# Optimization experiments

Hardware: AMD Instinct MI355X
Metric: run time of the kernel (lower is better)

The kernel has to match this reference:

```python
import jax, jax.numpy as jnp
import numpy as np

D_MODEL = 1024
NUM_HEADS = 16
HEAD_DIM = D_MODEL // NUM_HEADS
EPS = 1e-06


def setup_inputs() -> dict:
    key = jax.random.key(0)
    ks = jax.random.split(key, 7)
    B, T, D = 4, 4096, D_MODEL
    scale = 1.0 / np.sqrt(D)
    x = jax.random.normal(ks[0], (B, T, D), dtype=jnp.float32)
    Wq = jax.random.normal(ks[1], (D, D), dtype=jnp.float32) * scale
    Wk = jax.random.normal(ks[2], (D, D), dtype=jnp.float32) * scale
    Wv = jax.random.normal(ks[3], (D, D), dtype=jnp.float32) * scale
    Wo = jax.random.normal(ks[4], (D, D), dtype=jnp.float32) * scale
    Wg = jax.random.normal(ks[5], (D, D), dtype=jnp.float32) * scale
    bg = jnp.zeros((D,), dtype=jnp.float32)
    return {"x": x, "Wq": Wq, "Wk": Wk, "Wv": Wv, "Wo": Wo, "Wg": Wg, "bg": bg}


def phi(x):
    return jax.nn.elu(x) + 1.0


def reference(x, Wq, Wk, Wv, Wo, Wg, bg):
    B, T, D = x.shape
    H, Hd = NUM_HEADS, HEAD_DIM
    # torch nn.Linear: y = x @ W.T
    q = phi((x @ Wq.T).reshape(B, T, H, Hd))
    k = phi((x @ Wk.T).reshape(B, T, H, Hd))
    v = (x @ Wv.T).reshape(B, T, H, Hd)
    k_sum = k.sum(axis=1)                              # [B,H,Hd]
    kv_sum = jnp.einsum('bthd,bthd->bhd', k, v)        # [B,H,Hd] (elementwise-product reduction, as in source)
    # out[b,t,h,v] = sum_d q[b,t,h,d]*kv_sum[b,h,d], identical for every v
    s = jnp.einsum('bthd,bhd->bth', q, kv_sum)         # [B,T,H]
    z = jnp.einsum('bthd,bhd->bth', q, k_sum) + EPS    # [B,T,H]
    out = (s / z)[..., None] * jnp.ones((Hd,), dtype=x.dtype)  # broadcast over head_dim
    out = out.reshape(B, T, D)
    gate = jax.nn.sigmoid(x @ Wg.T + bg)
    return gate * out + (1.0 - gate) * x
```

## Files before the change

### kernel.cpp

```cpp
#include <hip/hip_runtime.h>

#define D_MODEL 1024
#define TSEQ    4096
#define BATCH   4
#define MROWS   (BATCH * TSEQ)
#define KDIM    1024
#define NDIM    1024
#define EPSV    1e-6f

typedef __attribute__((ext_vector_type(8))) short short8;
typedef __attribute__((ext_vector_type(4))) float floatx4;

__device__ inline unsigned short f2bf(float f) {
  unsigned u = __float_as_uint(f);
  unsigned r = (u + 0x7FFFu + ((u >> 16) & 1u)) >> 16;
  return (unsigned short)r;
}
__device__ inline float bf2f(unsigned short h) {
  return __uint_as_float(((unsigned)h) << 16);
}
__device__ inline float phi_f(float x) { return x > 0.f ? x + 1.f : __expf(x); }

#define NX4 4194304
#define NW4 262144
#define NZ4 2048

__global__ __launch_bounds__(256) void prep_kernel(
    const float* __restrict__ x,  const float* __restrict__ wq,
    const float* __restrict__ wk, const float* __restrict__ wv,
    const float* __restrict__ wg,
    unsigned short* __restrict__ xb,  unsigned short* __restrict__ wqb,
    unsigned short* __restrict__ wkb, unsigned short* __restrict__ wvb,
    unsigned short* __restrict__ wgb, float* __restrict__ zbase)
{
  long i = (long)blockIdx.x * 256 + threadIdx.x;
  const float* src; unsigned short* dst; long j = i;
  if (j < NX4) { src = x; dst = xb; }
  else {
    j -= NX4;
    if (j < NW4) { src = wq; dst = wqb; }
    else { j -= NW4;
      if (j < NW4) { src = wk; dst = wkb; }
      else { j -= NW4;
        if (j < NW4) { src = wv; dst = wvb; }
        else { j -= NW4;
          if (j < NW4) { src = wg; dst = wgb; }
          else { j -= NW4;
            if (j < NZ4) { float4 zz = {0.f,0.f,0.f,0.f}; ((float4*)zbase)[j] = zz; }
            return;
          }
        }
      }
    }
  }
  float4 f = ((const float4*)src)[j];
  ushort4 o;
  o.x = f2bf(f.x); o.y = f2bf(f.y); o.z = f2bf(f.z); o.w = f2bf(f.w);
  ((ushort4*)dst)[j] = o;
}

#define BM 128
#define BN 128
#define BK 32

__global__ __launch_bounds__(256, 2) void gemm_kv_kernel(
    const unsigned short* __restrict__ A,
    const unsigned short* __restrict__ Wk, const unsigned short* __restrict__ Wv,
    float* __restrict__ ksum, float* __restrict__ kvsum)
{
  const int bn = blockIdx.x;
  const int bm = blockIdx.y;

  __shared__ __align__(16) unsigned short As[BM * BK];
  __shared__ __align__(16) unsigned short Bk[BN * BK];
  __shared__ __align__(16) unsigned short Bv[BN * BK];

  const int tid  = threadIdx.x;
  const int lane = tid & 63;
  const int w    = tid >> 6;
  const int wr   = (w >> 1) * 64;
  const int wc   = (w & 1) * 64;

  floatx4 ak[4][4], av[4][4];
#pragma unroll
  for (int i = 0; i < 4; i++)
#pragma unroll
    for (int j = 0; j < 4; j++) {
      floatx4 zz = {0.f,0.f,0.f,0.f}; ak[i][j] = zz; av[i][j] = zz;
    }

  const unsigned short* Ablk  = A  + (size_t)bm * BM * KDIM;
  const unsigned short* Bkblk = Wk + (size_t)bn * BN * KDIM;
  const unsigned short* Bvblk = Wv + (size_t)bn * BN * KDIM;

  const int la = lane & 15;
  const int lk = (lane >> 4) * 8;

  for (int kt = 0; kt < KDIM; kt += BK) {
    __syncthreads();
#pragma unroll
    for (int c = 0; c < 2; c++) {
      int f   = tid + c * 256;
      int row = f >> 2;
      int col = (f & 3) * 8;
      size_t goff = (size_t)row * KDIM + kt + col;
      __builtin_amdgcn_global_load_lds(
          (const __attribute__((address_space(1))) void*)(Ablk + goff),
          (__attribute__((address_space(3))) void*)(As + (size_t)f * 8), 16, 0, 0);
      __builtin_amdgcn_global_load_lds(
          (const __attribute__((address_space(1))) void*)(Bkblk + goff),
          (__attribute__((address_space(3))) void*)(Bk + (size_t)f * 8), 16, 0, 0);
      __builtin_amdgcn_global_load_lds(
          (const __attribute__((address_space(1))) void*)(Bvblk + goff),
          (__attribute__((address_space(3))) void*)(Bv + (size_t)f * 8), 16, 0, 0);
    }
    __syncthreads();

    short8 af[4], bk[4], bv[4];
#pragma unroll
    for (int i = 0; i < 4; i++) {
      af[i] = *(const short8*)&As[(wr + i * 16 + la) * BK + lk];
      bk[i] = *(const short8*)&Bk[(wc + i * 16 + la) * BK + lk];
      bv[i] = *(const short8*)&Bv[(wc + i * 16 + la) * BK + lk];
    }
#pragma unroll
    for (int i = 0; i < 4; i++)
#pragma unroll
      for (int j = 0; j < 4; j++) {
        ak[i][j] = __builtin_amdgcn_mfma_f32_16x16x32_bf16(af[i], bk[j], ak[i][j], 0, 0, 0);
        av[i][j] = __builtin_amdgcn_mfma_f32_16x16x32_bf16(af[i], bv[j], av[i][j], 0, 0, 0);
      }
  }

  const int b = bm >> 5;
  float kp[4] = {0.f,0.f,0.f,0.f};
  float vp[4] = {0.f,0.f,0.f,0.f};
#pragma unroll
  for (int j = 0; j < 4; j++)
#pragma unroll
    for (int i = 0; i < 4; i++)
#pragma unroll
      for (int r = 0; r < 4; r++) {
        float kk = phi_f(ak[i][j][r]);
        kp[j] += kk;
        vp[j] += kk * av[i][j][r];
      }
#pragma unroll
  for (int j = 0; j < 4; j++) {
    kp[j] += __shfl_xor(kp[j], 16, 64); kp[j] += __shfl_xor(kp[j], 32, 64);
    vp[j] += __shfl_xor(vp[j], 16, 64); vp[j] += __shfl_xor(vp[j], 32, 64);
  }
  if (lane < 16) {
#pragma unroll
    for (int j = 0; j < 4; j++) {
      int col = bn * BN + wc + j * 16 + lane;
      atomicAdd(ksum  + (size_t)b * D_MODEL + col, kp[j]);
      atomicAdd(kvsum + (size_t)b * D_MODEL + col, vp[j]);
    }
  }
}

__global__ __launch_bounds__(512) void gemm_qg_kernel(
    const unsigned short* __restrict__ A,
    const unsigned short* __restrict__ Wq, const unsigned short* __restrict__ Wg,
    const float* __restrict__ x, const float* __restrict__ bg,
    const float* __restrict__ ksum, const float* __restrict__ kvsum,
    float* __restrict__ out)
{
  const int bn = blockIdx.x;
  const int bm = blockIdx.y;

  __shared__ __align__(16) unsigned short As[BM * BK];
  __shared__ __align__(16) unsigned short Bq[BN * BK];
  __shared__ __align__(16) unsigned short Bg[BN * BK];
  __shared__ float o_lds[2 * BM];

  const int tid  = threadIdx.x;
  const int lane = tid & 63;
  const int w    = tid >> 6;
  const int is_g = w >> 2;
  const int wl   = w & 3;
  const int wr   = (wl >> 1) * 64;
  const int wc   = (wl & 1) * 64;

  floatx4 acc[4][4];
#pragma unroll
  for (int i = 0; i < 4; i++)
#pragma unroll
    for (int j = 0; j < 4; j++) { floatx4 zz = {0.f,0.f,0.f,0.f}; acc[i][j] = zz; }

  const unsigned short* Ablk  = A + (size_t)bm * BM * KDIM;
  const unsigned short* Bqblk = Wq + (size_t)bn * BN * KDIM;
  const unsigned short* Bgblk = Wg + (size_t)bn * BN * KDIM;

  const int la = lane & 15;
  const int lk = (lane >> 4) * 8;
  const unsigned short* Bsm = is_g ? Bg : Bq;

  for (int kt = 0; kt < KDIM; kt += BK) {
    __syncthreads();
    {
      int f   = tid;
      int row = f >> 2;
      int col = (f & 3) * 8;
      size_t goff = (size_t)row * KDIM + kt + col;
      __builtin_amdgcn_global_load_lds(
          (const __attribute__((address_space(1))) void*)(Ablk + goff),
          (__attribute__((address_space(3))) void*)(As + (size_t)f * 8), 16, 0, 0);
      __builtin_amdgcn_global_load_lds(
          (const __attribute__((address_space(1))) void*)(Bqblk + goff),
          (__attribute__((address_space(3))) void*)(Bq + (size_t)f * 8), 16, 0, 0);
      __builtin_amdgcn_global_load_lds(
          (const __attribute__((address_space(1))) void*)(Bgblk + goff),
          (__attribute__((address_space(3))) void*)(Bg + (size_t)f * 8), 16, 0, 0);
    }
    __syncthreads();

    short8 af[4], bfg[4];
#pragma unroll
    for (int i = 0; i < 4; i++) {
      af[i]  = *(const short8*)&As[(wr + i * 16 + la) * BK + lk];
      bfg[i] = *(const short8*)&Bsm[(wc + i * 16 + la) * BK + lk];
    }
#pragma unroll
    for (int i = 0; i < 4; i++)
#pragma unroll
      for (int j = 0; j < 4; j++)
        acc[i][j] = __builtin_amdgcn_mfma_f32_16x16x32_bf16(af[i], bfg[j], acc[i][j], 0, 0, 0);
  }

  const int b  = bm >> 5;
  const int ro = (lane >> 4) * 4;
  const int co = lane & 15;
  const int hl = wc >> 6;

  if (!is_g) {
    float kvv[4], ksv[4];
#pragma unroll
    for (int j = 0; j < 4; j++) {
      int col = bn * BN + wc + j * 16 + co;
      kvv[j] = kvsum[(size_t)b * D_MODEL + col];
      ksv[j] = ksum [(size_t)b * D_MODEL + col];
    }
#pragma unroll
    for (int i = 0; i < 4; i++)
#pragma unroll
      for (int r = 0; r < 4; r++) {
        float s = 0.f, z = 0.f;
#pragma unroll
        for (int j = 0; j < 4; j++) {
          float qq = phi_f(acc[i][j][r]);
          s += qq * kvv[j]; z += qq * ksv[j];
        }
#pragma unroll
        for (int m = 1; m < 16; m <<= 1) {
          s += __shfl_xor(s, m, 64);
          z += __shfl_xor(z, m, 64);
        }
        if (co == 0) o_lds[hl * BM + wr + i * 16 + ro + r] = s / (z + EPSV);
      }
  }
  __syncthreads();
  if (is_g) {
    float bgv[4];
#pragma unroll
    for (int j = 0; j < 4; j++) bgv[j] = bg[bn * BN + wc + j * 16 + co];
#pragma unroll
    for (int i = 0; i < 4; i++)
#pragma unroll
      for (int r = 0; r < 4; r++) {
        int rowl = wr + i * 16 + ro + r;
        int grow = bm * BM + rowl;
        float ov = o_lds[hl * BM + rowl];
#pragma unroll
        for (int j = 0; j < 4; j++) {
          int gcol = bn * BN + wc + j * 16 + co;
          float gt = 1.f / (1.f + __expf(-(acc[i][j][r] + bgv[j])));
          float xv = x[(size_t)grow * D_MODEL + gcol];
          out[(size_t)grow * D_MODEL + gcol] = gt * ov + (1.f - gt) * xv;
        }
      }
  }
}

extern "C" void kernel_launch(void* const* d_in, const int* in_sizes, int n_in,
                              void* d_out, int out_size, void* d_ws, size_t ws_size,
                              hipStream_t stream) {
  (void)in_sizes; (void)n_in; (void)out_size; (void)ws_size;
  const float* x  = (const float*)d_in[0];
  const float* Wq = (const float*)d_in[1];
  const float* Wk = (const float*)d_in[2];
  const float* Wv = (const float*)d_in[3];
  const float* Wg = (const float*)d_in[5];
  const float* bg = (const float*)d_in[6];
  float* out = (float*)d_out;

  char* ws = (char*)d_ws;
  const size_t xel = (size_t)MROWS * D_MODEL;
  const size_t wel = (size_t)NDIM * KDIM;
  unsigned short* xbf = (unsigned short*)ws; ws += xel * 2;
  unsigned short* wqb = (unsigned short*)ws; ws += wel * 2;
  unsigned short* wkb = (unsigned short*)ws; ws += wel * 2;
  unsigned short* wvb = (unsigned short*)ws; ws += wel * 2;
  unsigned short* wgb = (unsigned short*)ws; ws += wel * 2;
  float* ksum  = (float*)ws; ws += (size_t)BATCH * D_MODEL * 4;
  float* kvsum = (float*)ws; ws += (size_t)BATCH * D_MODEL * 4;

  const long total4 = (long)NX4 + 4L * NW4 + NZ4;
  prep_kernel<<<(int)((total4 + 255) / 256), 256, 0, stream>>>(
      x, Wq, Wk, Wv, Wg, xbf, wqb, wkb, wvb, wgb, ksum);

  dim3 g1(NDIM / BN, MROWS / BM);
  gemm_kv_kernel<<<g1, 256, 0, stream>>>(xbf, wkb, wvb, ksum, kvsum);

  dim3 g2(NDIM / BN, MROWS / BM);
  gemm_qg_kernel<<<g2, 512, 0, stream>>>(xbf, wqb, wgb, x, bg, ksum, kvsum, out);
}
```

Measured before the change: 297.1 us.

## Double-buffer LDS tiles in both GEMM kernels to overlap loads with MFMA

Both fused GEMM kernels now keep two LDS buffers and issue the direct global-to-LDS loads for the next K tile before computing on the current one. This hides global load latency behind MFMA work and drops one barrier per K step. The MFMA block is also wrapped in s_setprio raises. LDS use doubles (to about 48KB in the kv kernel), which may reduce occupancy under its two-blocks-per-CU launch bound.

```diff
diff --git a/kernel.cpp b/kernel.cpp
--- a/kernel.cpp
+++ b/kernel.cpp
@@ -20,6 +20,10 @@
   return __uint_as_float(((unsigned)h) << 16);
 }
 __device__ inline float phi_f(float x) { return x > 0.f ? x + 1.f : __expf(x); }
+
+#define GLD16(gp, lp) __builtin_amdgcn_global_load_lds( \
+    (const __attribute__((address_space(1))) void*)(gp), \
+    (__attribute__((address_space(3))) void*)(lp), 16, 0, 0)
 
 #define NX4 4194304
 #define NW4 262144
@@ -71,9 +75,9 @@
   const int bn = blockIdx.x;
   const int bm = blockIdx.y;
 
-  __shared__ __align__(16) unsigned short As[BM * BK];
-  __shared__ __align__(16) unsigned short Bk[BN * BK];
-  __shared__ __align__(16) unsigned short Bv[BN * BK];
+  __shared__ __align__(16) unsigned short As [2][BM * BK];
+  __shared__ __align__(16) unsigned short Bks[2][BN * BK];
+  __shared__ __align__(16) unsigned short Bvs[2][BN * BK];
 
   const int tid  = threadIdx.x;
   const int lane = tid & 63;
@@ -96,33 +100,28 @@
   const int la = lane & 15;
   const int lk = (lane >> 4) * 8;
 
-  for (int kt = 0; kt < KDIM; kt += BK) {
-    __syncthreads();
-#pragma unroll
-    for (int c = 0; c < 2; c++) {
-      int f   = tid + c * 256;
-      int row = f >> 2;
-      int col = (f & 3) * 8;
-      size_t goff = (size_t)row * KDIM + kt + col;
-      __builtin_amdgcn_global_load_lds(
-          (const __attribute__((address_space(1))) void*)(Ablk + goff),
-          (__attribute__((address_space(3))) void*)(As + (size_t)f * 8), 16, 0, 0);
-      __builtin_amdgcn_global_load_lds(
-          (const __attribute__((address_space(1))) void*)(Bkblk + goff),
-          (__attribute__((address_space(3))) void*)(Bk + (size_t)f * 8), 16, 0, 0);
-      __builtin_amdgcn_global_load_lds(
-          (const __attribute__((address_space(1))) void*)(Bvblk + goff),
-          (__attribute__((address_space(3))) void*)(Bv + (size_t)f * 8), 16, 0, 0);
-    }
-    __syncthreads();
-
+  const int f0 = tid;
+  const int f1 = tid + 256;
+  const int r0 = f0 >> 2, c0 = (f0 & 3) * 8;
+  const int r1 = f1 >> 2, c1 = (f1 & 3) * 8;
+
+  auto stage = [&](int buf, int kt) {
+    size_t g0 = (size_t)r0 * KDIM + kt + c0;
+    size_t g1 = (size_t)r1 * KDIM + kt + c1;
+    GLD16(Ablk  + g0, &As [buf][f0 * 8]); GLD16(Ablk  + g1, &As [buf][f1 * 8]);
+    GLD16(Bkblk + g0, &Bks[buf][f0 * 8]); GLD16(Bkblk + g1, &Bks[buf][f1 * 8]);
+    GLD16(Bvblk + g0, &Bvs[buf][f0 * 8]); GLD16(Bvblk + g1, &Bvs[buf][f1 * 8]);
+  };
+
+  auto compute = [&](int buf) {
     short8 af[4], bk[4], bv[4];
 #pragma unroll
     for (int i = 0; i < 4; i++) {
-      af[i] = *(const short8*)&As[(wr + i * 16 + la) * BK + lk];
-      bk[i] = *(const short8*)&Bk[(wc + i * 16 + la) * BK + lk];
-      bv[i] = *(const short8*)&Bv[(wc + i * 16 + la) * BK + lk];
-    }
+      af[i] = *(const short8*)&As [buf][(wr + i * 16 + la) * BK + lk];
+      bk[i] = *(const short8*)&Bks[buf][(wc + i * 16 + la) * BK + lk];
+      bv[i] = *(const short8*)&Bvs[buf][(wc + i * 16 + la) * BK + lk];
+    }
+    __builtin_amdgcn_s_setprio(1);
 #pragma unroll
     for (int i = 0; i < 4; i++)
 #pragma unroll
@@ -130,6 +129,18 @@
         ak[i][j] = __builtin_amdgcn_mfma_f32_16x16x32_bf16(af[i], bk[j], ak[i][j], 0, 0, 0);
         av[i][j] = __builtin_amdgcn_mfma_f32_16x16x32_bf16(af[i], bv[j], av[i][j], 0, 0, 0);
       }
+    __builtin_amdgcn_s_setprio(0);
+  };
+
+  stage(0, 0);
+  __syncthreads();
+  for (int kt = 0; kt < KDIM; kt += 2 * BK) {
+    stage(1, kt + BK);
+    compute(0);
+    __syncthreads();
+    if (kt + 2 * BK < KDIM) stage(0, kt + 2 * BK);
+    compute(1);
+    __syncthreads();
   }
 
   const int b = bm >> 5;
@@ -170,9 +181,9 @@
   const int bn = blockIdx.x;
   const int bm = blockIdx.y;
 
-  __shared__ __align__(16) unsigned short As[BM * BK];
-  __shared__ __align__(16) unsigned short Bq[BN * BK];
-  __shared__ __align__(16) unsigned short Bg[BN * BK];
+  __shared__ __align__(16) unsigned short As [2][BM * BK];
+  __shared__ __align__(16) unsigned short Bqs[2][BN * BK];
+  __shared__ __align__(16) unsigned short Bgs[2][BN * BK];
   __shared__ float o_lds[2 * BM];
 
   const int tid  = threadIdx.x;
@@ -195,38 +206,43 @@
 
   const int la = lane & 15;
   const int lk = (lane >> 4) * 8;
-  const unsigned short* Bsm = is_g ? Bg : Bq;
-
-  for (int kt = 0; kt < KDIM; kt += BK) {
-    __syncthreads();
-    {
-      int f   = tid;
-      int row = f >> 2;
-      int col = (f & 3) * 8;
-      size_t goff = (size_t)row * KDIM + kt + col;
-      __builtin_amdgcn_global_load_lds(
-          (const __attribute__((address_space(1))) void*)(Ablk + goff),
-          (__attribute__((address_space(3))) void*)(As + (size_t)f * 8), 16, 0, 0);
-      __builtin_amdgcn_global_load_lds(
-          (const __attribute__((address_space(1))) void*)(Bqblk + goff),
-          (__attribute__((address_space(3))) void*)(Bq + (size_t)f * 8), 16, 0, 0);
-      __builtin_amdgcn_global_load_lds(
-          (const __attribute__((address_space(1))) void*)(Bgblk + goff),
-          (__attribute__((address_space(3))) void*)(Bg + (size_t)f * 8), 16, 0, 0);
-    }
-    __syncthreads();
-
+
+  const int f  = tid;
+  const int rr = f >> 2, cc = (f & 3) * 8;
+
+  auto stage = [&](int buf, int kt) {
+    size_t g = (size_t)rr * KDIM + kt + cc;
+    GLD16(Ablk  + g, &As [buf][f * 8]);
+    GLD16(Bqblk + g, &Bqs[buf][f * 8]);
+    GLD16(Bgblk + g, &Bgs[buf][f * 8]);
+  };
+
+  auto compute = [&](int buf) {
+    const unsigned short* Bsm = is_g ? &Bgs[buf][0] : &Bqs[buf][0];
     short8 af[4], bfg[4];
 #pragma unroll
     for (int i = 0; i < 4; i++) {
-      af[i]  = *(const short8*)&As[(wr + i * 16 + la) * BK + lk];
+      af[i]  = *(const short8*)&As[buf][(wr + i * 16 + la) * BK + lk];
       bfg[i] = *(const short8*)&Bsm[(wc + i * 16 + la) * BK + lk];
     }
+    __builtin_amdgcn_s_setprio(1);
 #pragma unroll
     for (int i = 0; i < 4; i++)
 #pragma unroll
       for (int j = 0; j < 4; j++)
         acc[i][j] = __builtin_amdgcn_mfma_f32_16x16x32_bf16(af[i], bfg[j], acc[i][j], 0, 0, 0);
+    __builtin_amdgcn_s_setprio(0);
+  };
+
+  stage(0, 0);
+  __syncthreads();
+  for (int kt = 0; kt < KDIM; kt += 2 * BK) {
+    stage(1, kt + BK);
+    compute(0);
+    __syncthreads();
+    if (kt + 2 * BK < KDIM) stage(0, kt + 2 * BK);
+    compute(1);
+    __syncthreads();
   }
 
   const int b  = bm >> 5;
```

Result: no change. 293.1 us (-1.4%).

## Retile both GEMMs to 128x64 with BK=64, XOR-swizzled LDS and grid swizzle

Applied to the files above, without the earlier changes.

Both fused GEMM kernels move to 128x64 output tiles with BK=64, which halves the number of K-loop barriers. The LDS tiles get an XOR swizzle to avoid bank conflicts on fragment reads. The 1-D grid is remapped so consecutive blocks share weight columns and land on different XCDs, and s_setprio is raised around the MFMA bursts. The Q/G kernel drops to 256 threads with 3 blocks per CU. The narrower N tile means the A operand is loaded from memory twice as often across the grid.

```diff
diff --git a/kernel.cpp b/kernel.cpp
--- a/kernel.cpp
+++ b/kernel.cpp
@@ -16,10 +16,11 @@
   unsigned r = (u + 0x7FFFu + ((u >> 16) & 1u)) >> 16;
   return (unsigned short)r;
 }
-__device__ inline float bf2f(unsigned short h) {
-  return __uint_as_float(((unsigned)h) << 16);
-}
 __device__ inline float phi_f(float x) { return x > 0.f ? x + 1.f : __expf(x); }
+
+#define GLD16(gp, lp) __builtin_amdgcn_global_load_lds( \
+    (const __attribute__((address_space(1))) void*)(gp), \
+    (__attribute__((address_space(3))) void*)(lp), 16, 0, 0)
 
 #define NX4 4194304
 #define NW4 262144
@@ -60,83 +61,125 @@
 }
 
 #define BM 128
-#define BN 128
-#define BK 32
-
-__global__ __launch_bounds__(256, 2) void gemm_kv_kernel(
+#define BNH 64
+#define BK 64
+#define NSTEP (KDIM / BK)
+
+#define GRID_SWZ(bid, bn, bm) \
+  const int sw_ = ((bid) & 7) * 256 + ((bid) >> 3); \
+  const int bn = sw_ >> 7; \
+  const int bm = sw_ & 127;
+
+__global__ __launch_bounds__(256, 3) void gemm_kv_kernel(
     const unsigned short* __restrict__ A,
     const unsigned short* __restrict__ Wk, const unsigned short* __restrict__ Wv,
     float* __restrict__ ksum, float* __restrict__ kvsum)
 {
-  const int bn = blockIdx.x;
-  const int bm = blockIdx.y;
-
   __shared__ __align__(16) unsigned short As[BM * BK];
-  __shared__ __align__(16) unsigned short Bk[BN * BK];
-  __shared__ __align__(16) unsigned short Bv[BN * BK];
+  __shared__ __align__(16) unsigned short Bk[BNH * BK];
+  __shared__ __align__(16) unsigned short Bv[BNH * BK];
+
+  GRID_SWZ(blockIdx.x, bn, bm);
 
   const int tid  = threadIdx.x;
   const int lane = tid & 63;
   const int w    = tid >> 6;
-  const int wr   = (w >> 1) * 64;
-  const int wc   = (w & 1) * 64;
-
-  floatx4 ak[4][4], av[4][4];
+  const int wrow = (w >> 1) * 64;
+  const int wc   = (w & 1) * 32;
+  const int la   = lane & 15;
+  const int l4   = lane >> 4;
+
+  floatx4 ak[4][2], av[4][2];
 #pragma unroll
   for (int i = 0; i < 4; i++)
 #pragma unroll
-    for (int j = 0; j < 4; j++) {
+    for (int j = 0; j < 2; j++) {
       floatx4 zz = {0.f,0.f,0.f,0.f}; ak[i][j] = zz; av[i][j] = zz;
     }
 
-  const unsigned short* Ablk  = A  + (size_t)bm * BM * KDIM;
-  const unsigned short* Bkblk = Wk + (size_t)bn * BN * KDIM;
-  const unsigned short* Bvblk = Wv + (size_t)bn * BN * KDIM;
-
-  const int la = lane & 15;
-  const int lk = (lane >> 4) * 8;
+  const unsigned short* Ablk = A  + (size_t)bm * BM * KDIM;
+  const unsigned short* Bkb  = Wk + (size_t)bn * BNH * KDIM;
+  const unsigned short* Bvb  = Wv + (size_t)bn * BNH * KDIM;
+
+  int aoff[4], aL[4], boff[2], bL[2];
+#pragma unroll
+  for (int i = 0; i < 4; i++) {
+    int s = tid + i * 256; int r = s >> 3;
+    aoff[i] = r * KDIM + (((s & 7) ^ (r & 7)) << 3);
+    aL[i]   = s * 8;
+  }
+#pragma unroll
+  for (int i = 0; i < 2; i++) {
+    int s = tid + i * 256; int r = s >> 3;
+    boff[i] = r * KDIM + (((s & 7) ^ (r & 7)) << 3);
+    bL[i]   = s * 8;
+  }
+
+  const int sl0 = (0 * 4 + l4) ^ (la & 7);
+  const int sl1 = (1 * 4 + l4) ^ (la & 7);
+  const int aB0 = (wrow + la) * BK + sl0 * 8;
+  const int aB1 = (wrow + la) * BK + sl1 * 8;
+  const int bB0 = (wc + la) * BK + sl0 * 8;
+  const int bB1 = (wc + la) * BK + sl1 * 8;
 
   for (int kt = 0; kt < KDIM; kt += BK) {
     __syncthreads();
 #pragma unroll
-    for (int c = 0; c < 2; c++) {
-      int f   = tid + c * 256;
-      int row = f >> 2;
-      int col = (f & 3) * 8;
-      size_t goff = (size_t)row * KDIM + kt + col;
-      __builtin_amdgcn_global_load_lds(
-          (const __attribute__((address_space(1))) void*)(Ablk + goff),
-          (__attribute__((address_space(3))) void*)(As + (size_t)f * 8), 16, 0, 0);
-      __builtin_amdgcn_global_load_lds(
-          (const __attribute__((address_space(1))) void*)(Bkblk + goff),
-          (__attribute__((address_space(3))) void*)(Bk + (size_t)f * 8), 16, 0, 0);
-      __builtin_amdgcn_global_load_lds(
-          (const __attribute__((address_space(1))) void*)(Bvblk + goff),
-          (__attribute__((address_space(3))) void*)(Bv + (size_t)f * 8), 16, 0, 0);
+    for (int i = 0; i < 4; ++i) GLD16(Ablk + aoff[i] + kt, As + aL[i]);
+#pragma unroll
+    for (int i = 0; i < 2; ++i) {
+      GLD16(Bkb + boff[i] + kt, Bk + bL[i]);
+      GLD16(Bvb + boff[i] + kt, Bv + bL[i]);
     }
     __syncthreads();
 
-    short8 af[4], bk[4], bv[4];
-#pragma unroll
-    for (int i = 0; i < 4; i++) {
-      af[i] = *(const short8*)&As[(wr + i * 16 + la) * BK + lk];
-      bk[i] = *(const short8*)&Bk[(wc + i * 16 + la) * BK + lk];
-      bv[i] = *(const short8*)&Bv[(wc + i * 16 + la) * BK + lk];
-    }
-#pragma unroll
-    for (int i = 0; i < 4; i++)
-#pragma unroll
-      for (int j = 0; j < 4; j++) {
-        ak[i][j] = __builtin_amdgcn_mfma_f32_16x16x32_bf16(af[i], bk[j], ak[i][j], 0, 0, 0);
-        av[i][j] = __builtin_amdgcn_mfma_f32_16x16x32_bf16(af[i], bv[j], av[i][j], 0, 0, 0);
-      }
+    short8 bkf[2][2], bvf[2][2];
+#pragma unroll
+    for (int j = 0; j < 2; ++j) {
+      bkf[j][0] = *(const short8*)(Bk + bB0 + j * (16*BK));
+      bkf[j][1] = *(const short8*)(Bk + bB1 + j * (16*BK));
+      bvf[j][0] = *(const short8*)(Bv + bB0 + j * (16*BK));
+      bvf[j][1] = *(const short8*)(Bv + bB1 + j * (16*BK));
+    }
+    short8 afA[2][2], afB[2][2];
+#pragma unroll
+    for (int rp = 0; rp < 2; ++rp) {
+      afA[rp][0] = *(const short8*)(As + aB0 + rp * (16*BK));
+      afA[rp][1] = *(const short8*)(As + aB1 + rp * (16*BK));
+      afB[rp][0] = *(const short8*)(As + aB0 + (2+rp) * (16*BK));
+      afB[rp][1] = *(const short8*)(As + aB1 + (2+rp) * (16*BK));
+    }
+    __builtin_amdgcn_s_setprio(1);
+#pragma unroll
+    for (int rp = 0; rp < 2; ++rp)
+#pragma unroll
+      for (int j = 0; j < 2; ++j)
+#pragma unroll
+        for (int kk = 0; kk < 2; ++kk) {
+          ak[rp][j] = __builtin_amdgcn_mfma_f32_16x16x32_bf16(
+              afA[rp][kk], bkf[j][kk], ak[rp][j], 0, 0, 0);
+          av[rp][j] = __builtin_amdgcn_mfma_f32_16x16x32_bf16(
+              afA[rp][kk], bvf[j][kk], av[rp][j], 0, 0, 0);
+        }
+#pragma unroll
+    for (int rp = 0; rp < 2; ++rp)
+#pragma unroll
+      for (int j = 0; j < 2; ++j)
+#pragma unroll
+        for (int kk = 0; kk < 2; ++kk) {
+          ak[2+rp][j] = __builtin_amdgcn_mfma_f32_16x16x32_bf16(
+              afB[rp][kk], bkf[j][kk], ak[2+rp][j], 0, 0, 0);
+          av[2+rp][j] = __builtin_amdgcn_mfma_f32_16x16x32_bf16(
+              afB[rp][kk], bvf[j][kk], av[2+rp][j], 0, 0, 0);
+        }
+    __builtin_amdgcn_s_setprio(0);
   }
 
   const int b = bm >> 5;
-  float kp[4] = {0.f,0.f,0.f,0.f};
-  float vp[4] = {0.f,0.f,0.f,0.f};
-#pragma unroll
-  for (int j = 0; j < 4; j++)
+  float kp[2] = {0.f, 0.f};
+  float vp[2] = {0.f, 0.f};
+#pragma unroll
+  for (int j = 0; j < 2; j++)
 #pragma unroll
     for (int i = 0; i < 4; i++)
 #pragma unroll
@@ -146,42 +189,41 @@
         vp[j] += kk * av[i][j][r];
       }
 #pragma unroll
-  for (int j = 0; j < 4; j++) {
+  for (int j = 0; j < 2; j++) {
     kp[j] += __shfl_xor(kp[j], 16, 64); kp[j] += __shfl_xor(kp[j], 32, 64);
     vp[j] += __shfl_xor(vp[j], 16, 64); vp[j] += __shfl_xor(vp[j], 32, 64);
   }
   if (lane < 16) {
 #pragma unroll
-    for (int j = 0; j < 4; j++) {
-      int col = bn * BN + wc + j * 16 + lane;
+    for (int j = 0; j < 2; j++) {
+      int col = bn * BNH + wc + j * 16 + lane;
       atomicAdd(ksum  + (size_t)b * D_MODEL + col, kp[j]);
       atomicAdd(kvsum + (size_t)b * D_MODEL + col, vp[j]);
     }
   }
 }
 
-__global__ __launch_bounds__(512) void gemm_qg_kernel(
+__global__ __launch_bounds__(256, 3) void gemm_qg_kernel(
     const unsigned short* __restrict__ A,
     const unsigned short* __restrict__ Wq, const unsigned short* __restrict__ Wg,
     const float* __restrict__ x, const float* __restrict__ bg,
     const float* __restrict__ ksum, const float* __restrict__ kvsum,
     float* __restrict__ out)
 {
-  const int bn = blockIdx.x;
-  const int bm = blockIdx.y;
-
   __shared__ __align__(16) unsigned short As[BM * BK];
-  __shared__ __align__(16) unsigned short Bq[BN * BK];
-  __shared__ __align__(16) unsigned short Bg[BN * BK];
-  __shared__ float o_lds[2 * BM];
+  __shared__ __align__(16) unsigned short Bq[BNH * BK];
+  __shared__ __align__(16) unsigned short Bg[BNH * BK];
+  __shared__ float o_lds[BM];
+
+  GRID_SWZ(blockIdx.x, bn, bm);
 
   const int tid  = threadIdx.x;
   const int lane = tid & 63;
   const int w    = tid >> 6;
-  const int is_g = w >> 2;
-  const int wl   = w & 3;
-  const int wr   = (wl >> 1) * 64;
-  const int wc   = (wl & 1) * 64;
+  const int is_g = w >> 1;
+  const int wr   = (w & 1) * 64;
+  const int la   = lane & 15;
+  const int l4   = lane >> 4;
 
   floatx4 acc[4][4];
 #pragma unroll
@@ -189,56 +231,87 @@
 #pragma unroll
     for (int j = 0; j < 4; j++) { floatx4 zz = {0.f,0.f,0.f,0.f}; acc[i][j] = zz; }
 
-  const unsigned short* Ablk  = A + (size_t)bm * BM * KDIM;
-  const unsigned short* Bqblk = Wq + (size_t)bn * BN * KDIM;
-  const unsigned short* Bgblk = Wg + (size_t)bn * BN * KDIM;
-
-  const int la = lane & 15;
-  const int lk = (lane >> 4) * 8;
+  const unsigned short* Ablk = A  + (size_t)bm * BM * KDIM;
+  const unsigned short* Bqb  = Wq + (size_t)bn * BNH * KDIM;
+  const unsigned short* Bgb  = Wg + (size_t)bn * BNH * KDIM;
+
+  int aoff[4], aL[4], boff[2], bL[2];
+#pragma unroll
+  for (int i = 0; i < 4; i++) {
+    int s = tid + i * 256; int r = s >> 3;
+    aoff[i] = r * KDIM + (((s & 7) ^ (r & 7)) << 3);
+    aL[i]   = s * 8;
+  }
+#pragma unroll
+  for (int i = 0; i < 2; i++) {
+    int s = tid + i * 256; int r = s >> 3;
+    boff[i] = r * KDIM + (((s & 7) ^ (r & 7)) << 3);
+    bL[i]   = s * 8;
+  }
+
+  const int sl0 = (0 * 4 + l4) ^ (la & 7);
+  const int sl1 = (1 * 4 + l4) ^ (la & 7);
+  const int aB0 = (wr + la) * BK + sl0 * 8;
+  const int aB1 = (wr + la) * BK + sl1 * 8;
+  const int bB0 = la * BK + sl0 * 8;
+  const int bB1 = la * BK + sl1 * 8;
+
   const unsigned short* Bsm = is_g ? Bg : Bq;
 
   for (int kt = 0; kt < KDIM; kt += BK) {
     __syncthreads();
-    {
-      int f   = tid;
-      int row = f >> 2;
-      int col = (f & 3) * 8;
-      size_t goff = (size_t)row * KDIM + kt + col;
-      __builtin_amdgcn_global_load_lds(
-          (const __attribute__((address_space(1))) void*)(Ablk + goff),
-          (__attribute__((address_space(3))) void*)(As + (size_t)f * 8), 16, 0, 0);
-      __builtin_amdgcn_global_load_lds(
-          (const __attribute__((address_space(1))) void*)(Bqblk + goff),
-          (__attribute__((address_space(3))) void*)(Bq + (size_t)f * 8), 16, 0, 0);
-      __builtin_amdgcn_global_load_lds(
-          (const __attribute__((address_space(1))) void*)(Bgblk + goff),
-          (__attribute__((address_space(3))) void*)(Bg + (size_t)f * 8), 16, 0, 0);
+#pragma unroll
+    for (int i = 0; i < 4; ++i) GLD16(Ablk + aoff[i] + kt, As + aL[i]);
+#pragma unroll
+    for (int i = 0; i < 2; ++i) {
+      GLD16(Bqb + boff[i] + kt, Bq + bL[i]);
+      GLD16(Bgb + boff[i] + kt, Bg + bL[i]);
     }
     __syncthreads();
 
-    short8 af[4], bfg[4];
-#pragma unroll
-    for (int i = 0; i < 4; i++) {
-      af[i]  = *(const short8*)&As[(wr + i * 16 + la) * BK + lk];
-      bfg[i] = *(const short8*)&Bsm[(wc + i * 16 + la) * BK + lk];
-    }
-#pragma unroll
-    for (int i = 0; i < 4; i++)
-#pragma unroll
-      for (int j = 0; j < 4; j++)
-        acc[i][j] = __builtin_amdgcn_mfma_f32_16x16x32_bf16(af[i], bfg[j], acc[i][j], 0, 0, 0);
+    short8 bf[4][2];
+#pragma unroll
+    for (int j = 0; j < 4; ++j) {
+      bf[j][0] = *(const short8*)(Bsm + bB0 + j * (16*BK));
+      bf[j][1] = *(const short8*)(Bsm + bB1 + j * (16*BK));
+    }
+    short8 afA[2][2], afB[2][2];
+#pragma unroll
+    for (int rp = 0; rp < 2; ++rp) {
+      afA[rp][0] = *(const short8*)(As + aB0 + rp * (16*BK));
+      afA[rp][1] = *(const short8*)(As + aB1 + rp * (16*BK));
+      afB[rp][0] = *(const short8*)(As + aB0 + (2+rp) * (16*BK));
+      afB[rp][1] = *(const short8*)(As + aB1 + (2+rp) * (16*BK));
+    }
+    __builtin_amdgcn_s_setprio(1);
+#pragma unroll
+    for (int rp = 0; rp < 2; ++rp)
+#pragma unroll
+      for (int j = 0; j < 4; ++j)
+#pragma unroll
+        for (int kk = 0; kk < 2; ++kk)
+          acc[rp][j] = __builtin_amdgcn_mfma_f32_16x16x32_bf16(
+              afA[rp][kk], bf[j][kk], acc[rp][j], 0, 0, 0);
+#pragma unroll
+    for (int rp = 0; rp < 2; ++rp)
+#pragma unroll
+      for (int j = 0; j < 4; ++j)
+#pragma unroll
+        for (int kk = 0; kk < 2; ++kk)
+          acc[2+rp][j] = __builtin_amdgcn_mfma_f32_16x16x32_bf16(
+              afB[rp][kk], bf[j][kk], acc[2+rp][j], 0, 0, 0);
+    __builtin_amdgcn_s_setprio(0);
   }
 
   const int b  = bm >> 5;
-  const int ro = (lane >> 4) * 4;
-  const int co = lane & 15;
-  const int hl = wc >> 6;
+  const int ro = l4 * 4;
+  const int co = la;
 
   if (!is_g) {
     float kvv[4], ksv[4];
 #pragma unroll
     for (int j = 0; j < 4; j++) {
-      int col = bn * BN + wc + j * 16 + co;
+      int col = bn * BNH + j * 16 + co;
       kvv[j] = kvsum[(size_t)b * D_MODEL + col];
       ksv[j] = ksum [(size_t)b * D_MODEL + col];
     }
@@ -257,24 +330,24 @@
           s += __shfl_xor(s, m, 64);
           z += __shfl_xor(z, m, 64);
         }
-        if (co == 0) o_lds[hl * BM + wr + i * 16 + ro + r] = s / (z + EPSV);
+        if (co == 0) o_lds[wr + i * 16 + ro + r] = s / (z + EPSV);
       }
   }
   __syncthreads();
   if (is_g) {
     float bgv[4];
 #pragma unroll
-    for (int j = 0; j < 4; j++) bgv[j] = bg[bn * BN + wc + j * 16 + co];
+    for (int j = 0; j < 4; j++) bgv[j] = bg[bn * BNH + j * 16 + co];
 #pragma unroll
     for (int i = 0; i < 4; i++)
 #pragma unroll
       for (int r = 0; r < 4; r++) {
         int rowl = wr + i * 16 + ro + r;
         int grow = bm * BM + rowl;
-        float ov = o_lds[hl * BM + rowl];
+        float ov = o_lds[rowl];
 #pragma unroll
         for (int j = 0; j < 4; j++) {
-          int gcol = bn * BN + wc + j * 16 + co;
+          int gcol = bn * BNH + j * 16 + co;
           float gt = 1.f / (1.f + __expf(-(acc[i][j][r] + bgv[j])));
           float xv = x[(size_t)grow * D_MODEL + gcol];
           out[(size_t)grow * D_MODEL + gcol] = gt * ov + (1.f - gt) * xv;
@@ -310,9 +383,7 @@
   prep_kernel<<<(int)((total4 + 255) / 256), 256, 0, stream>>>(
       x, Wq, Wk, Wv, Wg, xbf, wqb, wkb, wvb, wgb, ksum);
 
-  dim3 g1(NDIM / BN, MROWS / BM);
-  gemm_kv_kernel<<<g1, 256, 0, stream>>>(xbf, wkb, wvb, ksum, kvsum);
-
-  dim3 g2(NDIM / BN, MROWS / BM);
-  gemm_qg_kernel<<<g2, 512, 0, stream>>>(xbf, wqb, wgb, x, bg, ksum, kvsum, out);
-}
+  gemm_kv_kernel<<<2048, 256, 0, stream>>>(xbf, wkb, wvb, ksum, kvsum);
+
+  gemm_qg_kernel<<<2048, 256, 0, stream>>>(xbf, wqb, wgb, x, bg, ksum, kvsum, out);
+}
```

New measurement: 312.2 us. 5.1% more time.

## Replace LDS-staged GEMMs with register double-buffered direct global loads and swizzled grids

Applied to the files above, without the earlier changes.

Both GEMM kernels drop shared-memory staging and per-K-step barriers. Each wave now loads its A and B fragments straight from global memory into registers, double-buffered over 64-wide K chunks. Tile shapes change: the KV kernel uses 128x64 tiles, and the QG kernel uses 256x64 tiles where each wave pair splits Q and G. Launch grids are 1D with a block-index swizzle to improve L2 reuse. This removes LDS traffic and sync overhead, but loses intra-block data sharing, so more global/L2 traffic and register pressure are the risk.

```diff
diff --git a/kernel.cpp b/kernel.cpp
--- a/kernel.cpp
+++ b/kernel.cpp
@@ -15,9 +15,6 @@
   unsigned u = __float_as_uint(f);
   unsigned r = (u + 0x7FFFu + ((u >> 16) & 1u)) >> 16;
   return (unsigned short)r;
-}
-__device__ inline float bf2f(unsigned short h) {
-  return __uint_as_float(((unsigned)h) << 16);
 }
 __device__ inline float phi_f(float x) { return x > 0.f ? x + 1.f : __expf(x); }
 
@@ -59,129 +56,115 @@
   ((ushort4*)dst)[j] = o;
 }
 
-#define BM 128
-#define BN 128
-#define BK 32
+
+#define LD4(S, P, kt) { _Pragma("unroll") for (int f_ = 0; f_ < 4; ++f_) { \
+    S[f_][0] = *(const short8*)((P) + (size_t)f_ * 16 * KDIM + (kt)); \
+    S[f_][1] = *(const short8*)((P) + (size_t)f_ * 16 * KDIM + (kt) + 32); } }
+#define LD2(S, P, kt) { _Pragma("unroll") for (int j_ = 0; j_ < 2; ++j_) { \
+    S[j_][0] = *(const short8*)((P) + (size_t)j_ * 16 * KDIM + (kt)); \
+    S[j_][1] = *(const short8*)((P) + (size_t)j_ * 16 * KDIM + (kt) + 32); } }
 
 __global__ __launch_bounds__(256, 2) void gemm_kv_kernel(
     const unsigned short* __restrict__ A,
     const unsigned short* __restrict__ Wk, const unsigned short* __restrict__ Wv,
     float* __restrict__ ksum, float* __restrict__ kvsum)
 {
-  const int bn = blockIdx.x;
-  const int bm = blockIdx.y;
-
-  __shared__ __align__(16) unsigned short As[BM * BK];
-  __shared__ __align__(16) unsigned short Bk[BN * BK];
-  __shared__ __align__(16) unsigned short Bv[BN * BK];
+  const int bid = blockIdx.x;
+  const int sw  = (bid & 7) * 256 + (bid >> 3);
+  const int bn  = sw >> 7;
+  const int bm  = sw & 127;
 
   const int tid  = threadIdx.x;
   const int lane = tid & 63;
   const int w    = tid >> 6;
-  const int wr   = (w >> 1) * 64;
-  const int wc   = (w & 1) * 64;
-
-  floatx4 ak[4][4], av[4][4];
+  const int wm   = w >> 1;
+  const int wn   = w & 1;
+  const int la   = lane & 15;
+  const int l4   = lane >> 4;
+
+  floatx4 ak[4][2], av[4][2];
 #pragma unroll
   for (int i = 0; i < 4; i++)
 #pragma unroll
-    for (int j = 0; j < 4; j++) {
+    for (int j = 0; j < 2; j++) {
       floatx4 zz = {0.f,0.f,0.f,0.f}; ak[i][j] = zz; av[i][j] = zz;
     }
 
-  const unsigned short* Ablk  = A  + (size_t)bm * BM * KDIM;
-  const unsigned short* Bkblk = Wk + (size_t)bn * BN * KDIM;
-  const unsigned short* Bvblk = Wv + (size_t)bn * BN * KDIM;
-
-  const int la = lane & 15;
-  const int lk = (lane >> 4) * 8;
-
-  for (int kt = 0; kt < KDIM; kt += BK) {
-    __syncthreads();
-#pragma unroll
-    for (int c = 0; c < 2; c++) {
-      int f   = tid + c * 256;
-      int row = f >> 2;
-      int col = (f & 3) * 8;
-      size_t goff = (size_t)row * KDIM + kt + col;
-      __builtin_amdgcn_global_load_lds(
-          (const __attribute__((address_space(1))) void*)(Ablk + goff),
-          (__attribute__((address_space(3))) void*)(As + (size_t)f * 8), 16, 0, 0);
-      __builtin_amdgcn_global_load_lds(
-          (const __attribute__((address_space(1))) void*)(Bkblk + goff),
-          (__attribute__((address_space(3))) void*)(Bk + (size_t)f * 8), 16, 0, 0);
-      __builtin_amdgcn_global_load_lds(
-          (const __attribute__((address_space(1))) void*)(Bvblk + goff),
-          (__attribute__((address_space(3))) void*)(Bv + (size_t)f * 8), 16, 0, 0);
-    }
-    __syncthreads();
-
-    short8 af[4], bk[4], bv[4];
-#pragma unroll
-    for (int i = 0; i < 4; i++) {
-      af[i] = *(const short8*)&As[(wr + i * 16 + la) * BK + lk];
-      bk[i] = *(const short8*)&Bk[(wc + i * 16 + la) * BK + lk];
-      bv[i] = *(const short8*)&Bv[(wc + i * 16 + la) * BK + lk];
-    }
-#pragma unroll
-    for (int i = 0; i < 4; i++)
-#pragma unroll
-      for (int j = 0; j < 4; j++) {
-        ak[i][j] = __builtin_amdgcn_mfma_f32_16x16x32_bf16(af[i], bk[j], ak[i][j], 0, 0, 0);
-        av[i][j] = __builtin_amdgcn_mfma_f32_16x16x32_bf16(af[i], bv[j], av[i][j], 0, 0, 0);
-      }
+  const unsigned short* Ab = A  + (size_t)(bm * 128 + wm * 64 + la) * KDIM + l4 * 8;
+  const unsigned short* Kb = Wk + (size_t)(bn * 64 + wn * 32 + la) * KDIM + l4 * 8;
+  const unsigned short* Vb = Wv + (size_t)(bn * 64 + wn * 32 + la) * KDIM + l4 * 8;
+
+  short8 a0[4][2], a1[4][2], k0[2][2], k1[2][2], v0[2][2], v1[2][2];
+
+#define FMA_KV(SA, SK, SV) { _Pragma("unroll") for (int f_ = 0; f_ < 4; ++f_) \
+    _Pragma("unroll") for (int j_ = 0; j_ < 2; ++j_) \
+    _Pragma("unroll") for (int kk_ = 0; kk_ < 2; ++kk_) { \
+      ak[f_][j_] = __builtin_amdgcn_mfma_f32_16x16x32_bf16( \
+          SA[f_][kk_], SK[j_][kk_], ak[f_][j_], 0, 0, 0); \
+      av[f_][j_] = __builtin_amdgcn_mfma_f32_16x16x32_bf16( \
+          SA[f_][kk_], SV[j_][kk_], av[f_][j_], 0, 0, 0); } }
+
+  LD4(a0, Ab, 0); LD2(k0, Kb, 0); LD2(v0, Vb, 0);
+  for (int kt = 0; kt < KDIM; kt += 128) {
+    LD4(a1, Ab, kt + 64); LD2(k1, Kb, kt + 64); LD2(v1, Vb, kt + 64);
+    FMA_KV(a0, k0, v0);
+    if (kt + 128 < KDIM) {
+      LD4(a0, Ab, kt + 128); LD2(k0, Kb, kt + 128); LD2(v0, Vb, kt + 128);
+    }
+    FMA_KV(a1, k1, v1);
   }
 
   const int b = bm >> 5;
-  float kp[4] = {0.f,0.f,0.f,0.f};
-  float vp[4] = {0.f,0.f,0.f,0.f};
-#pragma unroll
-  for (int j = 0; j < 4; j++)
-#pragma unroll
-    for (int i = 0; i < 4; i++)
+  float kp[2] = {0.f, 0.f};
+  float vp[2] = {0.f, 0.f};
+#pragma unroll
+  for (int j = 0; j < 2; j++)
+#pragma unroll
+    for (int f = 0; f < 4; f++)
 #pragma unroll
       for (int r = 0; r < 4; r++) {
-        float kk = phi_f(ak[i][j][r]);
+        float kk = phi_f(ak[f][j][r]);
         kp[j] += kk;
-        vp[j] += kk * av[i][j][r];
-      }
-#pragma unroll
-  for (int j = 0; j < 4; j++) {
+        vp[j] += kk * av[f][j][r];
+      }
+#pragma unroll
+  for (int j = 0; j < 2; j++) {
     kp[j] += __shfl_xor(kp[j], 16, 64); kp[j] += __shfl_xor(kp[j], 32, 64);
     vp[j] += __shfl_xor(vp[j], 16, 64); vp[j] += __shfl_xor(vp[j], 32, 64);
   }
   if (lane < 16) {
 #pragma unroll
-    for (int j = 0; j < 4; j++) {
-      int col = bn * BN + wc + j * 16 + lane;
+    for (int j = 0; j < 2; j++) {
+      int col = bn * 64 + wn * 32 + j * 16 + lane;
       atomicAdd(ksum  + (size_t)b * D_MODEL + col, kp[j]);
       atomicAdd(kvsum + (size_t)b * D_MODEL + col, vp[j]);
     }
   }
-}
-
-__global__ __launch_bounds__(512) void gemm_qg_kernel(
+#undef FMA_KV
+}
+
+__global__ __launch_bounds__(512, 2) void gemm_qg_kernel(
     const unsigned short* __restrict__ A,
     const unsigned short* __restrict__ Wq, const unsigned short* __restrict__ Wg,
     const float* __restrict__ x, const float* __restrict__ bg,
     const float* __restrict__ ksum, const float* __restrict__ kvsum,
     float* __restrict__ out)
 {
-  const int bn = blockIdx.x;
-  const int bm = blockIdx.y;
-
-  __shared__ __align__(16) unsigned short As[BM * BK];
-  __shared__ __align__(16) unsigned short Bq[BN * BK];
-  __shared__ __align__(16) unsigned short Bg[BN * BK];
-  __shared__ float o_lds[2 * BM];
+  __shared__ float o_lds[256];
+
+  const int bid = blockIdx.x;
+  const int sw  = (bid & 7) * 128 + (bid >> 3);
+  const int bn  = sw >> 6;
+  const int bm  = sw & 63;
 
   const int tid  = threadIdx.x;
   const int lane = tid & 63;
   const int w    = tid >> 6;
-  const int is_g = w >> 2;
-  const int wl   = w & 3;
-  const int wr   = (wl >> 1) * 64;
-  const int wc   = (wl & 1) * 64;
+  const int wm   = w >> 1;
+  const int is_g = w & 1;
+  const int la   = lane & 15;
+  const int l4   = lane >> 4;
+  const int wr   = wm * 64;
 
   floatx4 acc[4][4];
 #pragma unroll
@@ -189,67 +172,46 @@
 #pragma unroll
     for (int j = 0; j < 4; j++) { floatx4 zz = {0.f,0.f,0.f,0.f}; acc[i][j] = zz; }
 
-  const unsigned short* Ablk  = A + (size_t)bm * BM * KDIM;
-  const unsigned short* Bqblk = Wq + (size_t)bn * BN * KDIM;
-  const unsigned short* Bgblk = Wg + (size_t)bn * BN * KDIM;
-
-  const int la = lane & 15;
-  const int lk = (lane >> 4) * 8;
-  const unsigned short* Bsm = is_g ? Bg : Bq;
-
-  for (int kt = 0; kt < KDIM; kt += BK) {
-    __syncthreads();
-    {
-      int f   = tid;
-      int row = f >> 2;
-      int col = (f & 3) * 8;
-      size_t goff = (size_t)row * KDIM + kt + col;
-      __builtin_amdgcn_global_load_lds(
-          (const __attribute__((address_space(1))) void*)(Ablk + goff),
-          (__attribute__((address_space(3))) void*)(As + (size_t)f * 8), 16, 0, 0);
-      __builtin_amdgcn_global_load_lds(
-          (const __attribute__((address_space(1))) void*)(Bqblk + goff),
-          (__attribute__((address_space(3))) void*)(Bq + (size_t)f * 8), 16, 0, 0);
-      __builtin_amdgcn_global_load_lds(
-          (const __attribute__((address_space(1))) void*)(Bgblk + goff),
-          (__attribute__((address_space(3))) void*)(Bg + (size_t)f * 8), 16, 0, 0);
-    }
-    __syncthreads();
-
-    short8 af[4], bfg[4];
-#pragma unroll
-    for (int i = 0; i < 4; i++) {
-      af[i]  = *(const short8*)&As[(wr + i * 16 + la) * BK + lk];
-      bfg[i] = *(const short8*)&Bsm[(wc + i * 16 + la) * BK + lk];
-    }
-#pragma unroll
-    for (int i = 0; i < 4; i++)
-#pragma unroll
-      for (int j = 0; j < 4; j++)
-        acc[i][j] = __builtin_amdgcn_mfma_f32_16x16x32_bf16(af[i], bfg[j], acc[i][j], 0, 0, 0);
-  }
-
-  const int b  = bm >> 5;
-  const int ro = (lane >> 4) * 4;
-  const int co = lane & 15;
-  const int hl = wc >> 6;
+  const unsigned short* Ab = A + (size_t)(bm * 256 + wr + la) * KDIM + l4 * 8;
+  const unsigned short* Wsel = is_g ? Wg : Wq;
+  const unsigned short* Bb = Wsel + (size_t)(bn * 64 + la) * KDIM + l4 * 8;
+
+  short8 a0[4][2], a1[4][2], b0[4][2], b1[4][2];
+
+#define FMA_QG(SA, SB) { _Pragma("unroll") for (int f_ = 0; f_ < 4; ++f_) \
+    _Pragma("unroll") for (int j_ = 0; j_ < 4; ++j_) \
+    _Pragma("unroll") for (int kk_ = 0; kk_ < 2; ++kk_) { \
+      acc[f_][j_] = __builtin_amdgcn_mfma_f32_16x16x32_bf16( \
+          SA[f_][kk_], SB[j_][kk_], acc[f_][j_], 0, 0, 0); } }
+
+  LD4(a0, Ab, 0); LD4(b0, Bb, 0);
+  for (int kt = 0; kt < KDIM; kt += 128) {
+    LD4(a1, Ab, kt + 64); LD4(b1, Bb, kt + 64);
+    FMA_QG(a0, b0);
+    if (kt + 128 < KDIM) { LD4(a0, Ab, kt + 128); LD4(b0, Bb, kt + 128); }
+    FMA_QG(a1, b1);
+  }
+
+  const int b  = bm >> 4;
+  const int ro = l4 * 4;
+  const int co = la;
 
   if (!is_g) {
     float kvv[4], ksv[4];
 #pragma unroll
     for (int j = 0; j < 4; j++) {
-      int col = bn * BN + wc + j * 16 + co;
+      int col = bn * 64 + j * 16 + co;
       kvv[j] = kvsum[(size_t)b * D_MODEL + col];
       ksv[j] = ksum [(size_t)b * D_MODEL + col];
     }
 #pragma unroll
-    for (int i = 0; i < 4; i++)
+    for (int f = 0; f < 4; f++)
 #pragma unroll
       for (int r = 0; r < 4; r++) {
         float s = 0.f, z = 0.f;
 #pragma unroll
         for (int j = 0; j < 4; j++) {
-          float qq = phi_f(acc[i][j][r]);
+          float qq = phi_f(acc[f][j][r]);
           s += qq * kvv[j]; z += qq * ksv[j];
         }
 #pragma unroll
@@ -257,30 +219,31 @@
           s += __shfl_xor(s, m, 64);
           z += __shfl_xor(z, m, 64);
         }
-        if (co == 0) o_lds[hl * BM + wr + i * 16 + ro + r] = s / (z + EPSV);
+        if (co == 0) o_lds[wr + f * 16 + ro + r] = s / (z + EPSV);
       }
   }
   __syncthreads();
   if (is_g) {
     float bgv[4];
 #pragma unroll
-    for (int j = 0; j < 4; j++) bgv[j] = bg[bn * BN + wc + j * 16 + co];
-#pragma unroll
-    for (int i = 0; i < 4; i++)
+    for (int j = 0; j < 4; j++) bgv[j] = bg[bn * 64 + j * 16 + co];
+#pragma unroll
+    for (int f = 0; f < 4; f++)
 #pragma unroll
       for (int r = 0; r < 4; r++) {
-        int rowl = wr + i * 16 + ro + r;
-        int grow = bm * BM + rowl;
-        float ov = o_lds[hl * BM + rowl];
+        int rowl = wr + f * 16 + ro + r;
+        int grow = bm * 256 + rowl;
+        float ov = o_lds[rowl];
 #pragma unroll
         for (int j = 0; j < 4; j++) {
-          int gcol = bn * BN + wc + j * 16 + co;
-          float gt = 1.f / (1.f + __expf(-(acc[i][j][r] + bgv[j])));
+          int gcol = bn * 64 + j * 16 + co;
+          float gt = 1.f / (1.f + __expf(-(acc[f][j][r] + bgv[j])));
           float xv = x[(size_t)grow * D_MODEL + gcol];
           out[(size_t)grow * D_MODEL + gcol] = gt * ov + (1.f - gt) * xv;
         }
       }
   }
+#undef FMA_QG
 }
 
 extern "C" void kernel_launch(void* const* d_in, const int* in_sizes, int n_in,
@@ -310,9 +273,7 @@
   prep_kernel<<<(int)((total4 + 255) / 256), 256, 0, stream>>>(
       x, Wq, Wk, Wv, Wg, xbf, wqb, wkb, wvb, wgb, ksum);
 
-  dim3 g1(NDIM / BN, MROWS / BM);
-  gemm_kv_kernel<<<g1, 256, 0, stream>>>(xbf, wkb, wvb, ksum, kvsum);
-
-  dim3 g2(NDIM / BN, MROWS / BM);
-  gemm_qg_kernel<<<g2, 512, 0, stream>>>(xbf, wqb, wgb, x, bg, ksum, kvsum, out);
-}
+  gemm_kv_kernel<<<2048, 256, 0, stream>>>(xbf, wkb, wvb, ksum, kvsum);
+
+  gemm_qg_kernel<<<1024, 512, 0, stream>>>(xbf, wqb, wgb, x, bg, ksum, kvsum, out);
+}
```

Measured after the change: 643.2 us. 2.16x slower.
